# Optimization experiments

Measured on AMD Instinct MI355X. Metric: run time of the kernel, lower is better.

## Reference

```python
import jax, jax.numpy as jnp
import numpy as np

NUM_CLASSES = 80
IGNORE = 0.5
LABEL_SMOOTH = 0.0
MAX_GT = 20
C = 5 + NUM_CLASSES
SIZES = (13, 26, 52)
BS = 64
ANCHORS = jnp.array([
    [[0.0240, 0.0313], [0.0385, 0.0721], [0.0793, 0.0553]],
    [[0.0721, 0.1466], [0.1490, 0.1082], [0.1418, 0.2861]],
    [[0.2788, 0.2163], [0.3750, 0.4760], [0.8966, 0.7837]],
], dtype=jnp.float32)
ANCH_REV = ANCHORS[::-1]  # anchors[[2,1,0]] in the torch code


def bce(p, t):
    p = jnp.clip(p, 1e-7, 1.0 - 1e-7)
    return -t * jnp.log(p) - (1.0 - t) * jnp.log(1.0 - p)


def cal_iou(b1, b2):
    tl = jnp.maximum(b1[..., 0:2] - b1[..., 2:4] / 2, b2[..., 0:2] - b2[..., 2:4] / 2)
    br = jnp.minimum(b1[..., 0:2] + b1[..., 2:4] / 2, b2[..., 0:2] + b2[..., 2:4] / 2)
    wh = jnp.maximum(br - tl, 0.0)
    inter = wh[..., 0] * wh[..., 1]
    union = b1[..., 2] * b1[..., 3] + b2[..., 2] * b2[..., 3] - inter
    return inter / jnp.clip(union, 1e-6)


def _sample_loss(preds, tflat):
    # preds: [N, C] decoded (x,y,w,h,conf,cls...); tflat: [M, C] target grid flattened
    N = preds.shape[0]
    conf_t = tflat[:, 4]
    _, idx = jax.lax.top_k(conf_t, MAX_GT)      # gather up to MAX_GT GT slots
    gts = tflat[idx]                            # [K, C]
    gmask = gts[:, 4]                           # 1.0 for real GT, 0.0 for padding
    iou = cal_iou(gts[:, None, :4], preds[None, :, :4])  # [K, N]
    best = jnp.argmax(iou, axis=-1)             # [K]
    sel = preds[best]                           # [K, C]
    reg = jnp.sum((sel[:, :4] - gts[:, :4]) ** 2, axis=-1) * (2.0 - gts[:, 2] * gts[:, 3])
    loss_reg = jnp.sum(gmask * reg)
    tar_cls = gts[:, 5:] * (1.0 - LABEL_SMOOTH) + LABEL_SMOOTH / NUM_CLASSES
    loss_cls = jnp.sum(gmask[:, None] * bce(sel[:, 5:], tar_cls))
    # noobj mask: zero at best-matched preds (valid GTs only) and at high-IoU preds
    noobj = jnp.ones(N, preds.dtype).at[best].multiply(1.0 - gmask)
    maxiou = jnp.max(iou * gmask[:, None], axis=0)  # [N]
    noobj = noobj * (maxiou < IGNORE).astype(preds.dtype)
    loss_conf = jnp.sum(gmask * bce(sel[:, 4], 1.0)) + jnp.sum(noobj * bce(preds[:, 4], 0.0))
    return loss_reg + loss_conf + loss_cls


def _scale_loss(pred, tgt, l):
    bs, lsz = pred.shape[0], pred.shape[-1]
    p = pred.reshape(bs, 3, C, lsz, lsz).transpose(0, 1, 3, 4, 2)  # [bs,3,h,w,C]
    raw_w, raw_h = p[..., 2], p[..., 3]
    s = jax.nn.sigmoid(p)
    grid = jnp.arange(lsz, dtype=p.dtype)
    x = (grid[None, None, None, :] + s[..., 0]) / lsz
    y = (grid[None, None, :, None] + s[..., 1]) / lsz
    anch = ANCH_REV[l]  # [3,2]
    w = anch[:, 0][None, :, None, None] * jnp.exp(raw_w)
    h = anch[:, 1][None, :, None, None] * jnp.exp(raw_h)
    boxes = jnp.stack([x, y, w, h], axis=-1)
    preds = jnp.concatenate([boxes, s[..., 4:5], s[..., 5:]], axis=-1).reshape(bs, -1, C)
    tflat = tgt.reshape(bs, -1, C)
    return jnp.sum(jax.vmap(_sample_loss)(preds, tflat))


def setup_inputs() -> dict:
    key = jax.random.key(0)
    ks = jax.random.split(key, 6)
    inp = {}
    for i, lsz in enumerate(SIZES):
        inp['pred%d' % i] = jax.random.normal(ks[i], (BS, 3 * C, lsz, lsz), dtype=jnp.float32)
        M = 3 * lsz * lsz
        kb, ki, kc = jax.random.split(ks[3 + i], 3)
        xywh = jax.random.uniform(kb, (BS, MAX_GT, 4), minval=0.05, maxval=0.6, dtype=jnp.float32)
        cls_idx = jax.random.randint(kc, (BS, MAX_GT), 0, NUM_CLASSES)
        entry = jnp.concatenate([xywh, jnp.ones((BS, MAX_GT, 1), jnp.float32),
                                 jax.nn.one_hot(cls_idx, NUM_CLASSES, dtype=jnp.float32)], axis=-1)
        pos = jax.random.randint(ki, (BS, MAX_GT), 0, M)
        tflat = jnp.zeros((BS, M, C), jnp.float32).at[jnp.arange(BS)[:, None], pos].set(entry)
        inp['targets%d' % i] = tflat.reshape(BS, 3, lsz, lsz, C)
    return inp


def reference(pred0, pred1, pred2, targets0, targets1, targets2):
    return (_scale_loss(pred0, targets0, 0)
            + _scale_loss(pred1, targets1, 1)
            + _scale_loss(pred2, targets2, 2))
```

## Files before the change

### kernel.cpp

```cpp
#include <hip/hip_runtime.h>

#define CC 85
#define NC 80
#define MAXGT 20
#define BSZ 64
#define IGNORE_T 0.5f
#define BT 512
#define NWAVE (BT/64)

__constant__ float d_anch[3][3][2] = {
  {{0.2788f,0.2163f},{0.375f,0.476f},{0.8966f,0.7837f}},
  {{0.0721f,0.1466f},{0.149f,0.1082f},{0.1418f,0.2861f}},
  {{0.024f,0.0313f},{0.0385f,0.0721f},{0.0793f,0.0553f}},
};

__device__ __forceinline__ float sigmoidf(float x){ return 1.0f/(1.0f+__expf(-x)); }
__device__ __forceinline__ float bcef(float p, float t){
  p = fminf(fmaxf(p, 1e-7f), 1.0f-1e-7f);
  return -t*__logf(p) - (1.0f-t)*__logf(1.0f-p);
}

struct SlotSmem {
  int cnt;
  int pos[MAXGT];
  int bn[MAXGT];
  float gx[MAXGT], gy[MAXGT], gw[MAXGT], gh[MAXGT];
  float4 tb[MAXGT];
  float area[MAXGT];
  unsigned long long lkey[NWAVE][MAXGT];
  float lnob[NWAVE];
  float lloss[NWAVE];
};

template<int LSZ, int S>
__device__ __forceinline__ void slot_loss(const float* __restrict__ pred,
                                          const float* __restrict__ tgt,
                                          float* __restrict__ out_slot,
                                          SlotSmem& sm)
{
  constexpr int L2 = LSZ*LSZ;
  constexpr int N  = 3*L2;
  const int tid = threadIdx.x;

  if (tid == 0) sm.cnt = 0;
  __syncthreads();
  for (int n = tid; n < N; n += BT) {
    if (tgt[(size_t)n*CC + 4] > 0.5f) {
      int i = atomicAdd(&sm.cnt, 1);
      if (i < MAXGT) sm.pos[i] = n;
    }
  }
  __syncthreads();
  const int G = min(sm.cnt, MAXGT);

  if (tid < MAXGT) {
    float x=0.f,y=0.f,w=0.f,h=0.f;
    if (tid < G) {
      const float* r = tgt + (size_t)sm.pos[tid]*CC;
      x=r[0]; y=r[1]; w=r[2]; h=r[3];
    }
    sm.gx[tid]=x; sm.gy[tid]=y; sm.gw[tid]=w; sm.gh[tid]=h;
    sm.tb[tid] = make_float4(x-w*0.5f, y-h*0.5f, x+w*0.5f, y+h*0.5f);
    sm.area[tid] = w*h;
  }
  __syncthreads();

  unsigned long long key[MAXGT];
  #pragma unroll
  for (int g=0; g<MAXGT; g++) key[g]=0ull;
  float noobj = 0.0f;
  const float inv = 1.0f/(float)LSZ;

  for (int base = 0; base < N; base += BT*4) {
    float rx0[4],rx1[4],ry0[4],ry1[4],pa[4],q4v[4],maxi[4];
    int nr[4];
    #pragma unroll
    for (int r=0;r<4;r++){
      const int n = base + r*BT + tid;
      nr[r]=n; maxi[r]=0.f;
      if (n < N) {
        const int a = n/L2, rem = n - a*L2;
        const int ii = rem/LSZ, jj = rem - ii*LSZ;
        const float* bp = pred + (size_t)a*CC*L2 + rem;
        const float q0=bp[0], q1=bp[L2], q2=bp[2*L2], q3=bp[3*L2];
        q4v[r]=bp[4*L2];
        const float px = ((float)jj + sigmoidf(q0))*inv;
        const float py = ((float)ii + sigmoidf(q1))*inv;
        const float pw = d_anch[S][a][0]*__expf(q2);
        const float ph = d_anch[S][a][1]*__expf(q3);
        rx0[r]=px-pw*0.5f; rx1[r]=px+pw*0.5f;
        ry0[r]=py-ph*0.5f; ry1[r]=py+ph*0.5f;
        pa[r]=pw*ph;
      } else {
        rx0[r]=0.f; rx1[r]=0.f; ry0[r]=0.f; ry1[r]=0.f; pa[r]=0.f; q4v[r]=0.f;
      }
    }
    #pragma unroll
    for (int g=0; g<MAXGT; g++){
      const float4 tb = sm.tb[g];
      const float ga = sm.area[g];
      #pragma unroll
      for (int r=0;r<4;r++){
        const float w = fmaxf(fminf(tb.z,rx1[r]) - fmaxf(tb.x,rx0[r]), 0.0f);
        const float h = fmaxf(fminf(tb.w,ry1[r]) - fmaxf(tb.y,ry0[r]), 0.0f);
        const float inter = w*h;
        const float io = inter / fmaxf(ga + pa[r] - inter, 1e-6f);
        maxi[r] = fmaxf(maxi[r], io);
        const unsigned long long k =
          ((unsigned long long)__float_as_uint(io)<<32) |
          (unsigned long long)(~(unsigned)nr[r]);
        if (k > key[g]) key[g] = k;
      }
    }
    #pragma unroll
    for (int r=0;r<4;r++)
      if (nr[r] < N && maxi[r] < IGNORE_T) noobj += bcef(sigmoidf(q4v[r]), 0.0f);
  }

  const int wid = tid>>6, lane = tid&63;
  #pragma unroll
  for (int g=0; g<MAXGT; g++){
    unsigned long long k = key[g];
    for (int off=32; off>0; off>>=1){
      const unsigned long long o = __shfl_down(k, off, 64);
      if (o > k) k = o;
    }
    if (lane==0) sm.lkey[wid][g] = k;
  }
  for (int off=32; off>0; off>>=1) noobj += __shfl_down(noobj, off, 64);
  if (lane==0) sm.lnob[wid] = noobj;
  __syncthreads();
  if (tid < MAXGT){
    unsigned long long k = sm.lkey[0][tid];
    #pragma unroll
    for (int w=1; w<NWAVE; w++){ const unsigned long long o = sm.lkey[w][tid]; if (o>k) k=o; }
    sm.bn[tid] = (int)(~(unsigned)(k & 0xffffffffull));
  }
  __syncthreads();

  float loss = 0.0f;
  if (tid < G){
    const int n = sm.bn[tid];
    const int a = n/L2, rem = n - a*L2, i = rem/LSZ, j = rem - i*LSZ;
    const float* bp = pred + (size_t)a*CC*L2 + rem;
    const float q0=bp[0], q1=bp[L2], q2=bp[2*L2], q3=bp[3*L2], q4=bp[4*L2];
    const float px = ((float)j + sigmoidf(q0))*inv;
    const float py = ((float)i + sigmoidf(q1))*inv;
    const float pw = d_anch[S][a][0]*__expf(q2);
    const float ph = d_anch[S][a][1]*__expf(q3);
    const float dx=px-sm.gx[tid], dy=py-sm.gy[tid], dw=pw-sm.gw[tid], dh=ph-sm.gh[tid];
    loss += (dx*dx+dy*dy+dw*dw+dh*dh)*(2.0f - sm.gw[tid]*sm.gh[tid]);
    loss += bcef(sigmoidf(q4), 1.0f);
    bool first = true;
    for (int g2=0; g2<tid; g2++) if (sm.bn[g2]==n) first=false;
    if (first){
      float maxiou = 0.0f;
      const float bx0=px-pw*0.5f, bx1=px+pw*0.5f, by0=py-ph*0.5f, by1=py+ph*0.5f;
      const float parea=pw*ph;
      for (int g2=0; g2<MAXGT; g2++){
        const float4 tb = sm.tb[g2];
        const float w = fmaxf(fminf(tb.z,bx1) - fmaxf(tb.x,bx0), 0.0f);
        const float h = fmaxf(fminf(tb.w,by1) - fmaxf(tb.y,by0), 0.0f);
        const float inter = w*h;
        maxiou = fmaxf(maxiou, inter / fmaxf(sm.area[g2]+parea-inter, 1e-6f));
      }
      if (maxiou < IGNORE_T) loss -= bcef(sigmoidf(q4), 0.0f);
    }
  }
  for (int idx = tid; idx < G*NC; idx += BT){
    const int g = idx/NC, c = idx - g*NC;
    const int n = sm.bn[g];
    const int a = n/L2, rem = n - a*L2;
    const float q  = pred[(size_t)a*CC*L2 + (size_t)(5+c)*L2 + rem];
    const float tc = tgt[(size_t)sm.pos[g]*CC + 5 + c];
    loss += bcef(sigmoidf(q), tc);
  }
  for (int off=32; off>0; off>>=1) loss += __shfl_down(loss, off, 64);
  if (lane==0) sm.lloss[wid] = loss;
  __syncthreads();
  if (tid==0){
    float v = 0.f;
    #pragma unroll
    for (int w=0; w<NWAVE; w++) v += sm.lloss[w] + sm.lnob[w];
    *out_slot = v;
  }
}

__global__ __launch_bounds__(BT, 2)
void k_fused(const float* __restrict__ p0, const float* __restrict__ t0,
             const float* __restrict__ p1, const float* __restrict__ t1,
             const float* __restrict__ p2, const float* __restrict__ t2,
             float* __restrict__ slot_out)
{
  __shared__ SlotSmem sm;
  const int b = blockIdx.x, s = blockIdx.y;
  float* o = slot_out + s*BSZ + b;
  if (s==0)      slot_loss<13,0>(p0 + (size_t)b*3*CC*13*13, t0 + (size_t)b*3*13*13*CC, o, sm);
  else if (s==1) slot_loss<26,1>(p1 + (size_t)b*3*CC*26*26, t1 + (size_t)b*3*26*26*CC, o, sm);
  else           slot_loss<52,2>(p2 + (size_t)b*3*CC*52*52, t2 + (size_t)b*3*52*52*CC, o, sm);
}

__global__ __launch_bounds__(256)
void k_sum(const float* __restrict__ slot_in, float* __restrict__ out)
{
  const int tid = threadIdx.x;
  float v = (tid < 3*BSZ) ? slot_in[tid] : 0.0f;
  for (int off=32; off>0; off>>=1) v += __shfl_down(v, off, 64);
  __shared__ float w[4];
  if ((tid&63)==0) w[tid>>6] = v;
  __syncthreads();
  if (tid==0) out[0] = w[0]+w[1]+w[2]+w[3];
}

extern "C" void kernel_launch(void* const* d_in, const int* in_sizes, int n_in,
                              void* d_out, int out_size, void* d_ws, size_t ws_size,
                              hipStream_t stream)
{
  const float* p0 = (const float*)d_in[0];
  const float* t0 = (const float*)d_in[1];
  const float* p1 = (const float*)d_in[2];
  const float* t1 = (const float*)d_in[3];
  const float* p2 = (const float*)d_in[4];
  const float* t2 = (const float*)d_in[5];
  float* slot = (float*)d_ws;

  k_fused<<<dim3(BSZ,3), BT, 0, stream>>>(p0,t0,p1,t1,p2,t2, slot);
  k_sum  <<<1, 256, 0, stream>>>(slot, (float*)d_out);
}
```

Before: 421.0 us.

## Split fused loss kernel into scan, chunked IoU, and final stages for more parallelism

The single per-(batch,scale) block kernel is replaced by four stages. A grid-wide scan finds GT slots with atomics into workspace. A chunked IoU kernel splits each sample's predictions into 1024-element chunks across more blocks and writes per-chunk argmax keys and noobj partial sums. A final kernel merges the keys and computes the regression and class losses split over two z-blocks. The aim is to fix load imbalance and low occupancy on the large 52x52 scale, since the old grid had only 192 blocks and the biggest scale dominated. The cost is extra launches, a memset, and global workspace round-trips.

```diff
diff --git a/kernel.cpp b/kernel.cpp
--- a/kernel.cpp
+++ b/kernel.cpp
@@ -5,8 +5,25 @@
 #define MAXGT 20
 #define BSZ 64
 #define IGNORE_T 0.5f
-#define BT 512
-#define NWAVE (BT/64)
+#define CHUNK 1024
+#define NCHMAX 8
+
+#define N0 507
+#define N1 2028
+#define N2 8112
+#define R0 (BSZ*N0)
+#define R1 (BSZ*N1)
+#define R2 (BSZ*N2)
+#define RTOT (R0+R1+R2)
+
+#define CNT_B    (192u*4u)
+#define POS_OFF  CNT_B
+#define POS_B    (192u*MAXGT*4u)
+#define KEY_OFF  (POS_OFF+POS_B)
+#define KEY_B    (192u*NCHMAX*MAXGT*8u)
+#define NOB_OFF  (KEY_OFF+KEY_B)
+#define NOB_B    (192u*NCHMAX*4u)
+#define PART_OFF (NOB_OFF+NOB_B)
 
 __constant__ float d_anch[3][3][2] = {
   {{0.2788f,0.2163f},{0.375f,0.476f},{0.8966f,0.7837f}},
@@ -20,103 +37,91 @@
   return -t*__logf(p) - (1.0f-t)*__logf(1.0f-p);
 }
 
-struct SlotSmem {
-  int cnt;
-  int pos[MAXGT];
-  int bn[MAXGT];
-  float gx[MAXGT], gy[MAXGT], gw[MAXGT], gh[MAXGT];
-  float4 tb[MAXGT];
-  float area[MAXGT];
-  unsigned long long lkey[NWAVE][MAXGT];
-  float lnob[NWAVE];
-  float lloss[NWAVE];
-};
+template<int N>
+__device__ __forceinline__ void scan_one(const float* __restrict__ tgt, int rl,
+                                         int s, int* __restrict__ cnt,
+                                         int* __restrict__ pos){
+  int b = rl / N;
+  int n = rl - b*N;
+  if (tgt[(size_t)rl*CC + 4] > 0.5f){
+    int slot = s*BSZ + b;
+    int i = atomicAdd(&cnt[slot], 1);
+    if (i < MAXGT) pos[slot*MAXGT + i] = n;
+  }
+}
+
+__global__ __launch_bounds__(256)
+void k_scan(const float* __restrict__ t0, const float* __restrict__ t1,
+            const float* __restrict__ t2,
+            int* __restrict__ cnt, int* __restrict__ pos){
+  int r = blockIdx.x*256 + threadIdx.x;
+  if (r < R0)         scan_one<N0>(t0, r,       0, cnt, pos);
+  else if (r < R0+R1) scan_one<N1>(t1, r-R0,    1, cnt, pos);
+  else if (r < RTOT)  scan_one<N2>(t2, r-R0-R1, 2, cnt, pos);
+}
 
 template<int LSZ, int S>
-__device__ __forceinline__ void slot_loss(const float* __restrict__ pred,
-                                          const float* __restrict__ tgt,
-                                          float* __restrict__ out_slot,
-                                          SlotSmem& sm)
-{
-  constexpr int L2 = LSZ*LSZ;
-  constexpr int N  = 3*L2;
+__device__ __forceinline__ void iou_one(const float* __restrict__ pred,
+                                        const float* __restrict__ tgt,
+                                        int b, int chunk,
+                                        const int* __restrict__ cnt,
+                                        const int* __restrict__ pos,
+                                        unsigned long long* __restrict__ keys,
+                                        float* __restrict__ nob){
+  constexpr int L2 = LSZ*LSZ, N = 3*L2;
+  const int n0 = chunk*CHUNK;
+  if (n0 >= N) return;
+  const int slot = S*BSZ + b;
+  const float* P = pred + (size_t)b*3*CC*L2;
+  const float* T = tgt  + (size_t)b*N*CC;
   const int tid = threadIdx.x;
-
-  if (tid == 0) sm.cnt = 0;
-  __syncthreads();
-  for (int n = tid; n < N; n += BT) {
-    if (tgt[(size_t)n*CC + 4] > 0.5f) {
-      int i = atomicAdd(&sm.cnt, 1);
-      if (i < MAXGT) sm.pos[i] = n;
-    }
-  }
-  __syncthreads();
-  const int G = min(sm.cnt, MAXGT);
-
-  if (tid < MAXGT) {
+  __shared__ float4 tb[MAXGT];
+  __shared__ float  area[MAXGT];
+  __shared__ unsigned long long lkey[4][MAXGT];
+  __shared__ float  lnob[4];
+  if (tid < MAXGT){
+    int G = min(cnt[slot], MAXGT);
     float x=0.f,y=0.f,w=0.f,h=0.f;
-    if (tid < G) {
-      const float* r = tgt + (size_t)sm.pos[tid]*CC;
+    if (tid < G){
+      const float* r = T + (size_t)pos[slot*MAXGT+tid]*CC;
       x=r[0]; y=r[1]; w=r[2]; h=r[3];
     }
-    sm.gx[tid]=x; sm.gy[tid]=y; sm.gw[tid]=w; sm.gh[tid]=h;
-    sm.tb[tid] = make_float4(x-w*0.5f, y-h*0.5f, x+w*0.5f, y+h*0.5f);
-    sm.area[tid] = w*h;
-  }
-  __syncthreads();
-
+    tb[tid]   = make_float4(x-w*0.5f, y-h*0.5f, x+w*0.5f, y+h*0.5f);
+    area[tid] = w*h;
+  }
+  __syncthreads();
   unsigned long long key[MAXGT];
   #pragma unroll
   for (int g=0; g<MAXGT; g++) key[g]=0ull;
   float noobj = 0.0f;
   const float inv = 1.0f/(float)LSZ;
-
-  for (int base = 0; base < N; base += BT*4) {
-    float rx0[4],rx1[4],ry0[4],ry1[4],pa[4],q4v[4],maxi[4];
-    int nr[4];
-    #pragma unroll
-    for (int r=0;r<4;r++){
-      const int n = base + r*BT + tid;
-      nr[r]=n; maxi[r]=0.f;
-      if (n < N) {
-        const int a = n/L2, rem = n - a*L2;
-        const int ii = rem/LSZ, jj = rem - ii*LSZ;
-        const float* bp = pred + (size_t)a*CC*L2 + rem;
-        const float q0=bp[0], q1=bp[L2], q2=bp[2*L2], q3=bp[3*L2];
-        q4v[r]=bp[4*L2];
-        const float px = ((float)jj + sigmoidf(q0))*inv;
-        const float py = ((float)ii + sigmoidf(q1))*inv;
-        const float pw = d_anch[S][a][0]*__expf(q2);
-        const float ph = d_anch[S][a][1]*__expf(q3);
-        rx0[r]=px-pw*0.5f; rx1[r]=px+pw*0.5f;
-        ry0[r]=py-ph*0.5f; ry1[r]=py+ph*0.5f;
-        pa[r]=pw*ph;
-      } else {
-        rx0[r]=0.f; rx1[r]=0.f; ry0[r]=0.f; ry1[r]=0.f; pa[r]=0.f; q4v[r]=0.f;
-      }
-    }
+  const int nend = min(n0+CHUNK, N);
+  for (int n = n0+tid; n < nend; n += 256){
+    const int a = n/L2, rem = n - a*L2, ii = rem/LSZ, jj = rem - ii*LSZ;
+    const float* bp = P + (size_t)a*CC*L2 + rem;
+    const float q0=bp[0], q1=bp[L2], q2=bp[2*L2], q3=bp[3*L2], q4=bp[4*L2];
+    const float px = ((float)jj + sigmoidf(q0))*inv;
+    const float py = ((float)ii + sigmoidf(q1))*inv;
+    const float pw = d_anch[S][a][0]*__expf(q2);
+    const float ph = d_anch[S][a][1]*__expf(q3);
+    const float x0=px-pw*0.5f, x1=px+pw*0.5f, y0=py-ph*0.5f, y1=py+ph*0.5f;
+    const float pa = pw*ph;
+    float maxi = 0.0f;
+    const unsigned long long nin = (unsigned long long)(~(unsigned)n);
     #pragma unroll
     for (int g=0; g<MAXGT; g++){
-      const float4 tb = sm.tb[g];
-      const float ga = sm.area[g];
-      #pragma unroll
-      for (int r=0;r<4;r++){
-        const float w = fmaxf(fminf(tb.z,rx1[r]) - fmaxf(tb.x,rx0[r]), 0.0f);
-        const float h = fmaxf(fminf(tb.w,ry1[r]) - fmaxf(tb.y,ry0[r]), 0.0f);
-        const float inter = w*h;
-        const float io = inter / fmaxf(ga + pa[r] - inter, 1e-6f);
-        maxi[r] = fmaxf(maxi[r], io);
-        const unsigned long long k =
-          ((unsigned long long)__float_as_uint(io)<<32) |
-          (unsigned long long)(~(unsigned)nr[r]);
-        if (k > key[g]) key[g] = k;
-      }
-    }
-    #pragma unroll
-    for (int r=0;r<4;r++)
-      if (nr[r] < N && maxi[r] < IGNORE_T) noobj += bcef(sigmoidf(q4v[r]), 0.0f);
-  }
-
+      const float4 t4 = tb[g];
+      const float w = fmaxf(fminf(t4.z,x1) - fmaxf(t4.x,x0), 0.0f);
+      const float h = fmaxf(fminf(t4.w,y1) - fmaxf(t4.y,y0), 0.0f);
+      const float inter = w*h;
+      const float io = inter / fmaxf(area[g]+pa-inter, 1e-6f);
+      maxi = fmaxf(maxi, io);
+      const unsigned long long k =
+        ((unsigned long long)__float_as_uint(io)<<32) | nin;
+      if (k > key[g]) key[g] = k;
+    }
+    if (maxi < IGNORE_T) noobj += bcef(sigmoidf(q4), 0.0f);
+  }
   const int wid = tid>>6, lane = tid&63;
   #pragma unroll
   for (int g=0; g<MAXGT; g++){
@@ -125,91 +130,147 @@
       const unsigned long long o = __shfl_down(k, off, 64);
       if (o > k) k = o;
     }
-    if (lane==0) sm.lkey[wid][g] = k;
+    if (lane==0) lkey[wid][g] = k;
   }
   for (int off=32; off>0; off>>=1) noobj += __shfl_down(noobj, off, 64);
-  if (lane==0) sm.lnob[wid] = noobj;
+  if (lane==0) lnob[wid] = noobj;
   __syncthreads();
   if (tid < MAXGT){
-    unsigned long long k = sm.lkey[0][tid];
-    #pragma unroll
-    for (int w=1; w<NWAVE; w++){ const unsigned long long o = sm.lkey[w][tid]; if (o>k) k=o; }
-    sm.bn[tid] = (int)(~(unsigned)(k & 0xffffffffull));
-  }
-  __syncthreads();
-
+    unsigned long long k = lkey[0][tid];
+    #pragma unroll
+    for (int w=1; w<4; w++){ const unsigned long long o = lkey[w][tid]; if (o>k) k=o; }
+    keys[((size_t)slot*NCHMAX + chunk)*MAXGT + tid] = k;
+  }
+  if (tid==0) nob[slot*NCHMAX + chunk] = lnob[0]+lnob[1]+lnob[2]+lnob[3];
+}
+
+__global__ __launch_bounds__(256, 2)
+void k_iou(const float* __restrict__ p0, const float* __restrict__ t0,
+           const float* __restrict__ p1, const float* __restrict__ t1,
+           const float* __restrict__ p2, const float* __restrict__ t2,
+           const int* __restrict__ cnt, const int* __restrict__ pos,
+           unsigned long long* __restrict__ keys, float* __restrict__ nob){
+  const int chunk = blockIdx.x, b = blockIdx.y, s = blockIdx.z;
+  if (s==0)      iou_one<13,0>(p0, t0, b, chunk, cnt, pos, keys, nob);
+  else if (s==1) iou_one<26,1>(p1, t1, b, chunk, cnt, pos, keys, nob);
+  else           iou_one<52,2>(p2, t2, b, chunk, cnt, pos, keys, nob);
+}
+
+template<int LSZ, int S, int NCH>
+__device__ __forceinline__ void final_one(const float* __restrict__ pred,
+                                          const float* __restrict__ tgt,
+                                          int b, int z,
+                                          const int* __restrict__ cnt,
+                                          const int* __restrict__ pos,
+                                          const unsigned long long* __restrict__ keys,
+                                          const float* __restrict__ nob,
+                                          float* __restrict__ part){
+  constexpr int L2 = LSZ*LSZ, N = 3*L2;
+  const int slot = S*BSZ + b;
+  const float* P = pred + (size_t)b*3*CC*L2;
+  const float* T = tgt  + (size_t)b*N*CC;
+  const int tid = threadIdx.x;
+  __shared__ int bn[MAXGT];
+  __shared__ int gp[MAXGT];
+  __shared__ float gx[MAXGT], gy[MAXGT], gw[MAXGT], gh[MAXGT];
+  __shared__ float4 tb[MAXGT];
+  __shared__ float area[MAXGT];
+  const int G = min(cnt[slot], MAXGT);
+  if (tid < MAXGT){
+    unsigned long long k = keys[((size_t)slot*NCHMAX + 0)*MAXGT + tid];
+    #pragma unroll
+    for (int c=1; c<NCH; c++){
+      const unsigned long long o = keys[((size_t)slot*NCHMAX + c)*MAXGT + tid];
+      if (o > k) k = o;
+    }
+    bn[tid] = (int)(~(unsigned)(k & 0xffffffffull));
+    float x=0.f,y=0.f,w=0.f,h=0.f; int p=0;
+    if (tid < G){
+      p = pos[slot*MAXGT + tid];
+      const float* r = T + (size_t)p*CC;
+      x=r[0]; y=r[1]; w=r[2]; h=r[3];
+    }
+    gp[tid]=p; gx[tid]=x; gy[tid]=y; gw[tid]=w; gh[tid]=h;
+    tb[tid]   = make_float4(x-w*0.5f, y-h*0.5f, x+w*0.5f, y+h*0.5f);
+    area[tid] = w*h;
+  }
+  __syncthreads();
   float loss = 0.0f;
-  if (tid < G){
-    const int n = sm.bn[tid];
+  const float inv = 1.0f/(float)LSZ;
+  if (z == 0 && tid < G){
+    const int n = bn[tid];
     const int a = n/L2, rem = n - a*L2, i = rem/LSZ, j = rem - i*LSZ;
-    const float* bp = pred + (size_t)a*CC*L2 + rem;
+    const float* bp = P + (size_t)a*CC*L2 + rem;
     const float q0=bp[0], q1=bp[L2], q2=bp[2*L2], q3=bp[3*L2], q4=bp[4*L2];
     const float px = ((float)j + sigmoidf(q0))*inv;
     const float py = ((float)i + sigmoidf(q1))*inv;
     const float pw = d_anch[S][a][0]*__expf(q2);
     const float ph = d_anch[S][a][1]*__expf(q3);
-    const float dx=px-sm.gx[tid], dy=py-sm.gy[tid], dw=pw-sm.gw[tid], dh=ph-sm.gh[tid];
-    loss += (dx*dx+dy*dy+dw*dw+dh*dh)*(2.0f - sm.gw[tid]*sm.gh[tid]);
+    const float dx=px-gx[tid], dy=py-gy[tid], dw=pw-gw[tid], dh=ph-gh[tid];
+    loss += (dx*dx+dy*dy+dw*dw+dh*dh)*(2.0f - gw[tid]*gh[tid]);
     loss += bcef(sigmoidf(q4), 1.0f);
     bool first = true;
-    for (int g2=0; g2<tid; g2++) if (sm.bn[g2]==n) first=false;
+    for (int g2=0; g2<tid; g2++) if (bn[g2]==n) first=false;
     if (first){
+      const float bx0=px-pw*0.5f, bx1=px+pw*0.5f, by0=py-ph*0.5f, by1=py+ph*0.5f;
+      const float parea = pw*ph;
       float maxiou = 0.0f;
-      const float bx0=px-pw*0.5f, bx1=px+pw*0.5f, by0=py-ph*0.5f, by1=py+ph*0.5f;
-      const float parea=pw*ph;
       for (int g2=0; g2<MAXGT; g2++){
-        const float4 tb = sm.tb[g2];
-        const float w = fmaxf(fminf(tb.z,bx1) - fmaxf(tb.x,bx0), 0.0f);
-        const float h = fmaxf(fminf(tb.w,by1) - fmaxf(tb.y,by0), 0.0f);
+        const float4 t4 = tb[g2];
+        const float w = fmaxf(fminf(t4.z,bx1) - fmaxf(t4.x,bx0), 0.0f);
+        const float h = fmaxf(fminf(t4.w,by1) - fmaxf(t4.y,by0), 0.0f);
         const float inter = w*h;
-        maxiou = fmaxf(maxiou, inter / fmaxf(sm.area[g2]+parea-inter, 1e-6f));
+        maxiou = fmaxf(maxiou, inter / fmaxf(area[g2]+parea-inter, 1e-6f));
       }
       if (maxiou < IGNORE_T) loss -= bcef(sigmoidf(q4), 0.0f);
     }
   }
-  for (int idx = tid; idx < G*NC; idx += BT){
+  if (z == 0 && tid == 0){
+    #pragma unroll
+    for (int c=0; c<NCH; c++) loss += nob[slot*NCHMAX + c];
+  }
+  for (int idx = z*256 + tid; idx < G*NC; idx += 512){
     const int g = idx/NC, c = idx - g*NC;
-    const int n = sm.bn[g];
+    const int n = bn[g];
     const int a = n/L2, rem = n - a*L2;
-    const float q  = pred[(size_t)a*CC*L2 + (size_t)(5+c)*L2 + rem];
-    const float tc = tgt[(size_t)sm.pos[g]*CC + 5 + c];
+    const float q  = P[(size_t)a*CC*L2 + (size_t)(5+c)*L2 + rem];
+    const float tc = T[(size_t)gp[g]*CC + 5 + c];
     loss += bcef(sigmoidf(q), tc);
   }
+  __shared__ float wsum[4];
   for (int off=32; off>0; off>>=1) loss += __shfl_down(loss, off, 64);
-  if (lane==0) sm.lloss[wid] = loss;
-  __syncthreads();
-  if (tid==0){
-    float v = 0.f;
-    #pragma unroll
-    for (int w=0; w<NWAVE; w++) v += sm.lloss[w] + sm.lnob[w];
-    *out_slot = v;
-  }
-}
-
-__global__ __launch_bounds__(BT, 2)
-void k_fused(const float* __restrict__ p0, const float* __restrict__ t0,
+  if ((tid&63)==0) wsum[tid>>6] = loss;
+  __syncthreads();
+  if (tid==0) part[slot*2 + z] = wsum[0]+wsum[1]+wsum[2]+wsum[3];
+}
+
+__global__ __launch_bounds__(256)
+void k_final(const float* __restrict__ p0, const float* __restrict__ t0,
              const float* __restrict__ p1, const float* __restrict__ t1,
              const float* __restrict__ p2, const float* __restrict__ t2,
-             float* __restrict__ slot_out)
-{
-  __shared__ SlotSmem sm;
-  const int b = blockIdx.x, s = blockIdx.y;
-  float* o = slot_out + s*BSZ + b;
-  if (s==0)      slot_loss<13,0>(p0 + (size_t)b*3*CC*13*13, t0 + (size_t)b*3*13*13*CC, o, sm);
-  else if (s==1) slot_loss<26,1>(p1 + (size_t)b*3*CC*26*26, t1 + (size_t)b*3*26*26*CC, o, sm);
-  else           slot_loss<52,2>(p2 + (size_t)b*3*CC*52*52, t2 + (size_t)b*3*52*52*CC, o, sm);
-}
-
-__global__ __launch_bounds__(256)
-void k_sum(const float* __restrict__ slot_in, float* __restrict__ out)
-{
+             const int* __restrict__ cnt, const int* __restrict__ pos,
+             const unsigned long long* __restrict__ keys,
+             const float* __restrict__ nob, float* __restrict__ part){
+  const int b = blockIdx.x, s = blockIdx.y, z = blockIdx.z;
+  if (s==0)      final_one<13,0,1>(p0, t0, b, z, cnt, pos, keys, nob, part);
+  else if (s==1) final_one<26,1,2>(p1, t1, b, z, cnt, pos, keys, nob, part);
+  else           final_one<52,2,8>(p2, t2, b, z, cnt, pos, keys, nob, part);
+}
+
+__global__ __launch_bounds__(384)
+void k_sum(const float* __restrict__ part, float* __restrict__ out){
   const int tid = threadIdx.x;
-  float v = (tid < 3*BSZ) ? slot_in[tid] : 0.0f;
+  float v = part[tid];
   for (int off=32; off>0; off>>=1) v += __shfl_down(v, off, 64);
-  __shared__ float w[4];
+  __shared__ float w[6];
   if ((tid&63)==0) w[tid>>6] = v;
   __syncthreads();
-  if (tid==0) out[0] = w[0]+w[1]+w[2]+w[3];
+  if (tid==0){
+    float s = 0.f;
+    #pragma unroll
+    for (int i=0; i<6; i++) s += w[i];
+    out[0] = s;
+  }
 }
 
 extern "C" void kernel_launch(void* const* d_in, const int* in_sizes, int n_in,
@@ -222,8 +283,19 @@
   const float* t1 = (const float*)d_in[3];
   const float* p2 = (const float*)d_in[4];
   const float* t2 = (const float*)d_in[5];
-  float* slot = (float*)d_ws;
-
-  k_fused<<<dim3(BSZ,3), BT, 0, stream>>>(p0,t0,p1,t1,p2,t2, slot);
-  k_sum  <<<1, 256, 0, stream>>>(slot, (float*)d_out);
-}
+  char* ws = (char*)d_ws;
+  int*                ws_cnt  = (int*)(ws);
+  int*                ws_pos  = (int*)(ws + POS_OFF);
+  unsigned long long* ws_keys = (unsigned long long*)(ws + KEY_OFF);
+  float*              ws_nob  = (float*)(ws + NOB_OFF);
+  float*              ws_part = (float*)(ws + PART_OFF);
+
+  hipMemsetAsync(ws_cnt, 0, CNT_B, stream);
+
+  k_scan <<<(RTOT+255)/256, 256, 0, stream>>>(t0,t1,t2, ws_cnt, ws_pos);
+  k_iou  <<<dim3(NCHMAX,BSZ,3), 256, 0, stream>>>(p0,t0,p1,t1,p2,t2,
+                                                  ws_cnt, ws_pos, ws_keys, ws_nob);
+  k_final<<<dim3(BSZ,3,2), 256, 0, stream>>>(p0,t0,p1,t1,p2,t2,
+                                             ws_cnt, ws_pos, ws_keys, ws_nob, ws_part);
+  k_sum  <<<1, 384, 0, stream>>>(ws_part, (float*)d_out);
+}
```

Measured after the change: 402.9 us. -4.3%, faster.
